# Kernel tuning notes

Measured on AMD Instinct MI355X. Metric: run time of the kernel, lower is better.

## Reference

```python
import jax, jax.numpy as jnp
import numpy as np

N_NODES = 50000
N_EDGES = 1_600_000
IN_DIM = 64
HID_DIM = 64
OUT_DIM = 64


def setup_inputs() -> dict:
    key = jax.random.key(0)
    k = jax.random.split(key, 7)
    feat = jax.random.normal(k[0], (N_NODES, IN_DIM), dtype=jnp.float32)
    src = jax.random.randint(k[1], (N_EDGES,), 0, N_NODES, dtype=jnp.int32)
    dst = jax.random.randint(k[2], (N_EDGES,), 0, N_NODES, dtype=jnp.int32)
    # nn.init.normal_(weight, std=0.1); bias default uniform ~ small, use 0.1*randn
    W1 = 0.1 * jax.random.normal(k[3], (HID_DIM, IN_DIM), dtype=jnp.float32)
    b1 = 0.1 * jax.random.normal(k[4], (HID_DIM,), dtype=jnp.float32)
    W2 = 0.1 * jax.random.normal(k[5], (OUT_DIM, HID_DIM), dtype=jnp.float32)
    b2 = 0.1 * jax.random.normal(k[6], (OUT_DIM,), dtype=jnp.float32)
    return {"feat": feat, "src": src, "dst": dst, "W1": W1, "b1": b1, "W2": W2, "b2": b2}


def _gnn_layer(h, src, dst, W, b):
    # copy_u + sum: gather source-node features along edges, scatter-sum to dst
    agg = jax.ops.segment_sum(h[src], dst, num_segments=N_NODES)  # [N, d_in]
    return agg @ W.T + b  # nn.Linear


def reference(feat, src, dst, W1, b1, W2, b2):
    h = _gnn_layer(feat, src, dst, W1, b1)
    h = jnp.tanh(h)
    h = _gnn_layer(h, src, dst, W2, b2)
    return h
```

## Files before the change

kernel.cpp:

```cpp
#include <hip/hip_runtime.h>

#define N_NODES 50000
#define N_EDGES 1600000
#define DIM 64
#define NBK 196
#define BIN_BLOCKS 391
#define CSR_CAP 12288
#define OCT_CAP 1536
#define QCAP 3072
#define GEMM_BLOCKS 197
#define NB_AGG8 6250

__device__ __forceinline__ unsigned short f2bf(float f) {
    union { float f; unsigned u; } v; v.f = f;
    unsigned r = v.u + 0x7FFF + ((v.u >> 16) & 1);
    return (unsigned short)(r >> 16);
}
__device__ __forceinline__ float bf2f(unsigned short h) {
    union { unsigned u; float f; } v; v.u = ((unsigned)h) << 16;  return v.f;
}
__device__ __forceinline__ float blo(unsigned u) {
    union { unsigned u; float f; } v; v.u = u << 16; return v.f;
}
__device__ __forceinline__ float bhi(unsigned u) {
    union { unsigned u; float f; } v; v.u = u & 0xFFFF0000u; return v.f;
}

__global__ __launch_bounds__(256) void bin_and_gemm1(const int* __restrict__ src,
                                                     const int* __restrict__ dst,
                                                     int* __restrict__ bcur,
                                                     int* __restrict__ binned,
                                                     const float* __restrict__ X,
                                                     const float* __restrict__ W,
                                                     unsigned short* __restrict__ T) {
    __shared__ int cnt[NBK];
    __shared__ int lofs[NBK];
    __shared__ int shiftv[NBK];
    __shared__ int sb[256];
    __shared__ int stag[4096];
    __shared__ unsigned char stb[4096];
    __shared__ float Ws[64 * 64];
    int tid = threadIdx.x;

    if (blockIdx.x >= BIN_BLOCKS) {
#pragma unroll
        for (int j = 0; j < 16; ++j) Ws[j * 256 + tid] = W[j * 256 + tid];
        __syncthreads();

        int n = (blockIdx.x - BIN_BLOCKS) * 256 + tid;
        if (n > N_NODES) return;
        ushort4* tp = (ushort4*)(T + (size_t)n * 64);
        if (n == N_NODES) {
            ushort4 z = {0, 0, 0, 0};
#pragma unroll
            for (int k = 0; k < 16; ++k) tp[k] = z;
            return;
        }

        float4 x[16];
        const float4* xp = (const float4*)(X + (size_t)n * 64);
#pragma unroll
        for (int k = 0; k < 16; ++k) x[k] = xp[k];

        for (int fg = 0; fg < 16; ++fg) {
            float r[4];
#pragma unroll
            for (int fi = 0; fi < 4; ++fi) {
                int f = fg * 4 + fi;
                float acc = 0.f;
#pragma unroll
                for (int k4 = 0; k4 < 16; ++k4) {
                    float4 w = *(const float4*)&Ws[f * 64 + k4 * 4];
                    float4 xv = x[k4];
                    acc += xv.x * w.x + xv.y * w.y + xv.z * w.z + xv.w * w.w;
                }
                r[fi] = acc;
            }
            ushort4 o;
            o.x = f2bf(r[0]); o.y = f2bf(r[1]); o.z = f2bf(r[2]); o.w = f2bf(r[3]);
            tp[fg] = o;
        }
        return;
    }

    if (tid < NBK) cnt[tid] = 0;
    __syncthreads();

    int base = blockIdx.x * 4096;
    int oct = blockIdx.x & 7;
    int nedge = N_EDGES - base;
    if (nedge > 4096) nedge = 4096;

    int myb[16], myr[16], myp[16];
#pragma unroll
    for (int i = 0; i < 16; ++i) {
        int e = base + i * 256 + tid;
        myb[i] = -1;
        if (e < N_EDGES) {
            int s = src[e], d = dst[e];
            int b = d >> 8;
            myb[i] = b;
            myp[i] = ((d & 255) << 16) | s;
            myr[i] = atomicAdd(&cnt[b], 1);
        }
    }
    __syncthreads();

    int c = (tid < NBK) ? cnt[tid] : 0;
    sb[tid] = c;
    __syncthreads();
    for (int off = 1; off < 256; off <<= 1) {
        int u = (tid >= off) ? sb[tid - off] : 0;
        __syncthreads();
        sb[tid] += u;
        __syncthreads();
    }
    if (tid < NBK) {
        lofs[tid] = sb[tid] - c;
        if (c) shiftv[tid] = tid * CSR_CAP + oct * OCT_CAP
                           + atomicAdd(&bcur[(tid * 8 + oct) * 16], c) - lofs[tid];
    }
    __syncthreads();

#pragma unroll
    for (int i = 0; i < 16; ++i) {
        if (myb[i] >= 0) {
            int idx = lofs[myb[i]] + myr[i];
            stag[idx] = myp[i];
            stb[idx] = (unsigned char)myb[i];
        }
    }
    __syncthreads();

    for (int i = tid; i < nedge; i += 256)
        binned[i + shiftv[stb[i]]] = stag[i];
}

__global__ __launch_bounds__(256) void build_csr(const int* __restrict__ binned,
                                                 const int* __restrict__ bcur,
                                                 unsigned* __restrict__ nodeinfo,
                                                 unsigned short* __restrict__ csr16) {
    __shared__ int cnt[64], cnt2[64], ofs[64], sb[64];
    __shared__ int mo[8];
    int tid = threadIdx.x;
    int b = blockIdx.x >> 2;
    int q = blockIdx.x & 3;
    int qbase = (b * 4 + q) * QCAP;
    if (tid < 64) { cnt[tid] = 0; cnt2[tid] = 0; }
    if (tid < 8) {
        int m = bcur[(b * 8 + tid) * 16];
        mo[tid] = m > OCT_CAP ? OCT_CAP : m;
    }
    __syncthreads();

    for (int oct = 0; oct < 8; ++oct) {
        int ibase = b * CSR_CAP + oct * OCT_CAP;
        int m = mo[oct];
        for (int i = tid; i < m; i += 256) {
            int dl = (binned[ibase + i] >> 16) & 255;
            if ((dl >> 6) == q) atomicAdd(&cnt[dl & 63], 1);
        }
    }
    __syncthreads();

    int v = 0, myc = 0;
    if (tid < 64) { myc = cnt[tid]; v = (myc + 15) & ~15; sb[tid] = v; }
    __syncthreads();
    for (int off = 1; off < 64; off <<= 1) {
        int u = (tid >= off && tid < 64) ? sb[tid - off] : 0;
        __syncthreads();
        if (tid < 64) sb[tid] += u;
        __syncthreads();
    }
    if (tid < 64) {
        int o = sb[tid] - v;
        ofs[tid] = o;
        int node = (b << 8) + (q << 6) + tid;
        if (node < N_NODES)
            nodeinfo[node] = ((unsigned)v << 23) | (unsigned)(qbase + o);
        for (int i = myc; i < v; ++i)
            csr16[qbase + o + i] = (unsigned short)N_NODES;
    }
    __syncthreads();

    for (int oct = 0; oct < 8; ++oct) {
        int ibase = b * CSR_CAP + oct * OCT_CAP;
        int m = mo[oct];
        for (int i = tid; i < m; i += 256) {
            int p = binned[ibase + i];
            int dl = (p >> 16) & 255;
            if ((dl >> 6) == q) {
                int r = atomicAdd(&cnt2[dl & 63], 1);
                csr16[qbase + ofs[dl & 63] + r] = (unsigned short)(p & 0xFFFF);
            }
        }
    }
}

#define ACC8(d)                                                     \
    a0 += blo(d.x); a1 += bhi(d.x); a2 += blo(d.y); a3 += bhi(d.y); \
    a4 += blo(d.z); a5 += bhi(d.z); a6 += blo(d.w); a7 += bhi(d.w);

__global__ __launch_bounds__(512) void agg_fuse1(const unsigned short* __restrict__ T,
                                                 const unsigned short* __restrict__ csr,
                                                 const unsigned* __restrict__ nodeinfo,
                                                 const float* __restrict__ b1,
                                                 const float* __restrict__ W2,
                                                 unsigned short* __restrict__ T2) {
    __shared__ __align__(16) float4 W2t4[1024];
    __shared__ __align__(16) float part[8][8][72];
    int tid = threadIdx.x;
    int w = tid >> 6;
    int lane = tid & 63;
    int g8 = lane >> 3;
    int fs = lane & 7;
    int node = blockIdx.x * 8 + w;

    for (int L4 = tid; L4 < 1024; L4 += 512) {
        int k4 = L4 >> 6, f = L4 & 63;
        W2t4[L4] = *(const float4*)(W2 + f * 64 + k4 * 4);
    }

    unsigned info = __builtin_nontemporal_load(nodeinfo + node);
    float bias = b1[lane];
    int pos = (int)(info & 0x7FFFFFu);
    int nch = (int)(info >> 23) >> 3;
    const unsigned short* ip = csr + pos + g8;
    const uint4* Tp = (const uint4*)T;
    float a0 = 0.f, a1 = 0.f, a2 = 0.f, a3 = 0.f, a4 = 0.f, a5 = 0.f, a6 = 0.f, a7 = 0.f;
    int c = 0;
    for (; c + 4 <= nch; c += 4) {
        int j0 = __builtin_nontemporal_load(ip + c * 8);
        int j1 = __builtin_nontemporal_load(ip + c * 8 + 8);
        int j2 = __builtin_nontemporal_load(ip + c * 8 + 16);
        int j3 = __builtin_nontemporal_load(ip + c * 8 + 24);
        uint4 d0 = Tp[j0 * 8 + fs];
        uint4 d1 = Tp[j1 * 8 + fs];
        uint4 d2 = Tp[j2 * 8 + fs];
        uint4 d3 = Tp[j3 * 8 + fs];
        ACC8(d0) ACC8(d1) ACC8(d2) ACC8(d3)
    }
    if (c < nch) {
        int j0 = __builtin_nontemporal_load(ip + c * 8);
        int j1 = __builtin_nontemporal_load(ip + c * 8 + 8);
        uint4 d0 = Tp[j0 * 8 + fs];
        uint4 d1 = Tp[j1 * 8 + fs];
        ACC8(d0) ACC8(d1)
    }
    float4 pa = {a0, a1, a2, a3};
    float4 pb = {a4, a5, a6, a7};
    *(float4*)&part[w][g8][fs * 8] = pa;
    *(float4*)&part[w][g8][fs * 8 + 4] = pb;
    __syncthreads();

    float acc = bias;
#pragma unroll
    for (int g = 0; g < 8; ++g) acc += part[w][g][lane];

    float e = __expf(2.f * acc);
    part[w][0][lane] = 1.f - 2.f / (e + 1.f);

    const float* hrow = &part[w][0][0];
    float tf = 0.f;
#pragma unroll
    for (int k4 = 0; k4 < 16; ++k4) {
        float4 hv = *(const float4*)(hrow + k4 * 4);
        float4 wv = W2t4[k4 * 64 + lane];
        tf += hv.x * wv.x + hv.y * wv.y + hv.z * wv.z + hv.w * wv.w;
    }
    T2[(size_t)node * DIM + lane] = f2bf(tf);

    if (blockIdx.x == 0 && tid < 64)
        T2[(size_t)N_NODES * DIM + tid] = 0;
}

__global__ __launch_bounds__(512) void agg_out(const unsigned short* __restrict__ T,
                                               const unsigned short* __restrict__ csr,
                                               const unsigned* __restrict__ nodeinfo,
                                               const float* __restrict__ bias,
                                               float* __restrict__ outp) {
    __shared__ __align__(16) float part[8][8][72];
    int tid = threadIdx.x;
    int w = tid >> 6;
    int lane = tid & 63;
    int g8 = lane >> 3;
    int fs = lane & 7;
    int node = blockIdx.x * 8 + w;

    unsigned info = __builtin_nontemporal_load(nodeinfo + node);
    float bv = bias[lane];
    int pos = (int)(info & 0x7FFFFFu);
    int nch = (int)(info >> 23) >> 3;
    const unsigned short* ip = csr + pos + g8;
    const uint4* Tp = (const uint4*)T;
    float a0 = 0.f, a1 = 0.f, a2 = 0.f, a3 = 0.f, a4 = 0.f, a5 = 0.f, a6 = 0.f, a7 = 0.f;
    int c = 0;
    for (; c + 4 <= nch; c += 4) {
        int j0 = __builtin_nontemporal_load(ip + c * 8);
        int j1 = __builtin_nontemporal_load(ip + c * 8 + 8);
        int j2 = __builtin_nontemporal_load(ip + c * 8 + 16);
        int j3 = __builtin_nontemporal_load(ip + c * 8 + 24);
        uint4 d0 = Tp[j0 * 8 + fs];
        uint4 d1 = Tp[j1 * 8 + fs];
        uint4 d2 = Tp[j2 * 8 + fs];
        uint4 d3 = Tp[j3 * 8 + fs];
        ACC8(d0) ACC8(d1) ACC8(d2) ACC8(d3)
    }
    if (c < nch) {
        int j0 = __builtin_nontemporal_load(ip + c * 8);
        int j1 = __builtin_nontemporal_load(ip + c * 8 + 8);
        uint4 d0 = Tp[j0 * 8 + fs];
        uint4 d1 = Tp[j1 * 8 + fs];
        ACC8(d0) ACC8(d1)
    }
    float4 pa = {a0, a1, a2, a3};
    float4 pb = {a4, a5, a6, a7};
    *(float4*)&part[w][g8][fs * 8] = pa;
    *(float4*)&part[w][g8][fs * 8 + 4] = pb;

    float acc = bv;
#pragma unroll
    for (int g = 0; g < 8; ++g) acc += part[w][g][lane];
    __builtin_nontemporal_store(acc, outp + (size_t)node * DIM + lane);
}

extern "C" void kernel_launch(void* const* d_in, const int* in_sizes, int n_in,
                              void* d_out, int out_size, void* d_ws, size_t ws_size,
                              hipStream_t stream) {
    const float* feat = (const float*)d_in[0];
    const int*   src  = (const int*)d_in[1];
    const int*   dst  = (const int*)d_in[2];
    const float* W1   = (const float*)d_in[3];
    const float* b1   = (const float*)d_in[4];
    const float* W2   = (const float*)d_in[5];
    const float* b2   = (const float*)d_in[6];
    float* out = (float*)d_out;

    int*            binned   = (int*)d_ws;
    unsigned short* csr16    = (unsigned short*)(binned + NBK * CSR_CAP);
    unsigned*       nodeinfo = (unsigned*)(csr16 + NBK * 4 * QCAP);
    int*            bcur     = (int*)(nodeinfo + N_NODES);
    unsigned short* t        = (unsigned short*)(bcur + NBK * 8 * 16 + 8);
    unsigned short* t2       = t + (size_t)(N_NODES + 1) * 64;

    (void)hipMemsetAsync(bcur, 0, NBK * 8 * 16 * sizeof(int), stream);
    bin_and_gemm1<<<BIN_BLOCKS + GEMM_BLOCKS, 256, 0, stream>>>(
        src, dst, bcur, binned, feat, W1, t);
    build_csr<<<NBK * 4, 256, 0, stream>>>(binned, bcur, nodeinfo, csr16);

    agg_fuse1<<<NB_AGG8, 512, 0, stream>>>(t, csr16, nodeinfo, b1, W2, t2);

    agg_out<<<NB_AGG8, 512, 0, stream>>>(t2, csr16, nodeinfo, b2, out);
}
```

Before: 226.9 us.

## Split node GEMM from edge binning and tile it with register-held weights

Moves the first-layer feature transform out of the fused binning kernel into its own launch. The new kernel stages 128 node rows in shared memory and has each lane keep one weight row in registers, computing four nodes per step and writing bf16 outputs in a coalesced per-lane pattern. The old version held a whole node row per thread and re-read shared weights, which put pressure on registers and shared memory. The cost is an extra kernel launch and losing the overlap between binning and GEMM inside a single grid.

```diff
diff --git a/kernel.cpp b/kernel.cpp
--- a/kernel.cpp
+++ b/kernel.cpp
@@ -8,7 +8,7 @@
 #define CSR_CAP 12288
 #define OCT_CAP 1536
 #define QCAP 3072
-#define GEMM_BLOCKS 197
+#define G1_BLOCKS 391
 #define NB_AGG8 6250
 
 __device__ __forceinline__ unsigned short f2bf(float f) {
@@ -26,62 +26,17 @@
     union { unsigned u; float f; } v; v.u = u & 0xFFFF0000u; return v.f;
 }
 
-__global__ __launch_bounds__(256) void bin_and_gemm1(const int* __restrict__ src,
-                                                     const int* __restrict__ dst,
-                                                     int* __restrict__ bcur,
-                                                     int* __restrict__ binned,
-                                                     const float* __restrict__ X,
-                                                     const float* __restrict__ W,
-                                                     unsigned short* __restrict__ T) {
+__global__ __launch_bounds__(256) void bin_edges(const int* __restrict__ src,
+                                                 const int* __restrict__ dst,
+                                                 int* __restrict__ bcur,
+                                                 int* __restrict__ binned) {
     __shared__ int cnt[NBK];
     __shared__ int lofs[NBK];
     __shared__ int shiftv[NBK];
     __shared__ int sb[256];
     __shared__ int stag[4096];
     __shared__ unsigned char stb[4096];
-    __shared__ float Ws[64 * 64];
-    int tid = threadIdx.x;
-
-    if (blockIdx.x >= BIN_BLOCKS) {
-#pragma unroll
-        for (int j = 0; j < 16; ++j) Ws[j * 256 + tid] = W[j * 256 + tid];
-        __syncthreads();
-
-        int n = (blockIdx.x - BIN_BLOCKS) * 256 + tid;
-        if (n > N_NODES) return;
-        ushort4* tp = (ushort4*)(T + (size_t)n * 64);
-        if (n == N_NODES) {
-            ushort4 z = {0, 0, 0, 0};
-#pragma unroll
-            for (int k = 0; k < 16; ++k) tp[k] = z;
-            return;
-        }
-
-        float4 x[16];
-        const float4* xp = (const float4*)(X + (size_t)n * 64);
-#pragma unroll
-        for (int k = 0; k < 16; ++k) x[k] = xp[k];
-
-        for (int fg = 0; fg < 16; ++fg) {
-            float r[4];
-#pragma unroll
-            for (int fi = 0; fi < 4; ++fi) {
-                int f = fg * 4 + fi;
-                float acc = 0.f;
-#pragma unroll
-                for (int k4 = 0; k4 < 16; ++k4) {
-                    float4 w = *(const float4*)&Ws[f * 64 + k4 * 4];
-                    float4 xv = x[k4];
-                    acc += xv.x * w.x + xv.y * w.y + xv.z * w.z + xv.w * w.w;
-                }
-                r[fi] = acc;
-            }
-            ushort4 o;
-            o.x = f2bf(r[0]); o.y = f2bf(r[1]); o.z = f2bf(r[2]); o.w = f2bf(r[3]);
-            tp[fg] = o;
-        }
-        return;
-    }
+    int tid = threadIdx.x;
 
     if (tid < NBK) cnt[tid] = 0;
     __syncthreads();
@@ -134,6 +89,55 @@
 
     for (int i = tid; i < nedge; i += 256)
         binned[i + shiftv[stb[i]]] = stag[i];
+}
+
+__global__ __launch_bounds__(256) void gemm1(const float* __restrict__ X,
+                                             const float* __restrict__ W,
+                                             unsigned short* __restrict__ T) {
+    __shared__ __align__(16) float4 xs[128 * 16];
+    int tid = threadIdx.x;
+    int w = tid >> 6, lane = tid & 63;
+    int nbase = blockIdx.x * 128;
+
+    float4 wreg[16];
+    const float4* wp = (const float4*)(W + lane * 64);
+#pragma unroll
+    for (int k4 = 0; k4 < 16; ++k4) wreg[k4] = wp[k4];
+
+    const float4* xg = (const float4*)X;
+    for (int L = tid; L < 2048; L += 256) {
+        int row = nbase + (L >> 4);
+        float4 v = {0.f, 0.f, 0.f, 0.f};
+        if (row < N_NODES) v = xg[(size_t)row * 16 + (L & 15)];
+        xs[L] = v;
+    }
+    __syncthreads();
+
+    for (int g = 0; g < 8; ++g) {
+        int n0 = w * 32 + g * 4;
+        float accA = 0.f, accB = 0.f, accC = 0.f, accD = 0.f;
+#pragma unroll
+        for (int k4 = 0; k4 < 16; ++k4) {
+            float4 w4 = wreg[k4];
+            float4 xA = xs[(n0 + 0) * 16 + k4];
+            float4 xB = xs[(n0 + 1) * 16 + k4];
+            float4 xC = xs[(n0 + 2) * 16 + k4];
+            float4 xD = xs[(n0 + 3) * 16 + k4];
+            accA += xA.x * w4.x + xA.y * w4.y + xA.z * w4.z + xA.w * w4.w;
+            accB += xB.x * w4.x + xB.y * w4.y + xB.z * w4.z + xB.w * w4.w;
+            accC += xC.x * w4.x + xC.y * w4.y + xC.z * w4.z + xC.w * w4.w;
+            accD += xD.x * w4.x + xD.y * w4.y + xD.z * w4.z + xD.w * w4.w;
+        }
+        int gn = nbase + n0;
+        unsigned short vA = (gn + 0 == N_NODES) ? (unsigned short)0 : f2bf(accA);
+        unsigned short vB = (gn + 1 == N_NODES) ? (unsigned short)0 : f2bf(accB);
+        unsigned short vC = (gn + 2 == N_NODES) ? (unsigned short)0 : f2bf(accC);
+        unsigned short vD = (gn + 3 == N_NODES) ? (unsigned short)0 : f2bf(accD);
+        if (gn + 0 <= N_NODES) T[(size_t)(gn + 0) * 64 + lane] = vA;
+        if (gn + 1 <= N_NODES) T[(size_t)(gn + 1) * 64 + lane] = vB;
+        if (gn + 2 <= N_NODES) T[(size_t)(gn + 2) * 64 + lane] = vC;
+        if (gn + 3 <= N_NODES) T[(size_t)(gn + 3) * 64 + lane] = vD;
+    }
 }
 
 __global__ __launch_bounds__(256) void build_csr(const int* __restrict__ binned,
@@ -344,8 +348,8 @@
     unsigned short* t2       = t + (size_t)(N_NODES + 1) * 64;
 
     (void)hipMemsetAsync(bcur, 0, NBK * 8 * 16 * sizeof(int), stream);
-    bin_and_gemm1<<<BIN_BLOCKS + GEMM_BLOCKS, 256, 0, stream>>>(
-        src, dst, bcur, binned, feat, W1, t);
+    bin_edges<<<BIN_BLOCKS, 256, 0, stream>>>(src, dst, bcur, binned);
+    gemm1<<<G1_BLOCKS, 256, 0, stream>>>(feat, W1, t);
     build_csr<<<NBK * 4, 256, 0, stream>>>(binned, bcur, nodeinfo, csr16);
 
     agg_fuse1<<<NB_AGG8, 512, 0, stream>>>(t, csr16, nodeinfo, b1, W2, t2);
```

Measured after the change: 227.6 us. About the same (+0.3%).
